# Performance work log

Hardware: AMD Instinct MI355X
Metric: run time of the kernel (lower is better)

## Reference

```python
import jax, jax.numpy as jnp
import numpy as np

H = 8          # n_heads
D = 1024       # dim_tgt == dim_mem
DQ = D // H    # per-head dim = 128
BN = 512       # LFFN bottleneck (hardcoded in module)
HID = 1024     # LFFN hidden (hardcoded in module)
B = 16
S_T = 1024     # target length
S_M = 2048     # memory length
SCALE = DQ ** 0.25  # module uses dim_q ** (1/4)
EPS = 1e-5


def _ln(x, g, b):
    m = jnp.mean(x, axis=-1, keepdims=True)
    v = jnp.mean(jnp.square(x - m), axis=-1, keepdims=True)
    return (x - m) * jax.lax.rsqrt(v + EPS) * g + b


def _mhla(xq, xk, xv, Wq, Wk, Wv, Wo, masked):
    # per-head projections: x [b,s,D] x W [H,D,DQ] -> [b,H,s,DQ]
    Q = jnp.einsum('bsq,hqd->bhsd', xq, Wq)
    K = jnp.einsum('bsq,hqd->bhsd', xk, Wk)
    V = jnp.einsum('bsq,hqd->bhsd', xv, Wv)
    if masked:
        s, d = Q.shape[-2], Q.shape[-1]
        # module adds log(triu(ones).T) directly to Q: 0 where d_idx<=t, -inf otherwise
        m = jnp.where(jnp.arange(d)[None, :] <= jnp.arange(s)[:, None], 0.0, -jnp.inf)
        Q = Q + m.astype(Q.dtype)
    # softmax_col(K^T/d_k) over head-dim axis == softmax(K/d_k, axis=-1)
    A = jnp.einsum('bhsd,bhse->bhde', jax.nn.softmax(K / SCALE, axis=-1), V)  # [b,H,DQ,DQ]
    Bm = jnp.einsum('bhsd,bhde->bhse', jax.nn.softmax(Q / SCALE, axis=-1), A)  # [b,H,s,DQ]
    b, h, w, dd = Bm.shape
    # torch .view(b, w, h*d) on contiguous [b,h,w,d]: raw row-major reshape (no transpose)
    Bm = Bm.reshape(b, w, h * dd)
    return Bm @ Wo.T


def setup_inputs():
    key = jax.random.key(0)
    ks = jax.random.split(key, 24)
    r = lambda k, sh, s=0.02: (jax.random.normal(k, sh, jnp.float32) * s)
    return {
        'mem': jax.random.normal(ks[0], (B, S_M, D), jnp.float32),
        'y': jax.random.normal(ks[1], (B, S_T, D), jnp.float32),
        # self-attention (masked)
        'Wq1': r(ks[2], (H, D, DQ)), 'Wk1': r(ks[3], (H, D, DQ)), 'Wv1': r(ks[4], (H, D, DQ)),
        'Wo1': r(ks[5], (D, D)),
        # cross-attention with memory
        'Wq2': r(ks[6], (H, D, DQ)), 'Wk2': r(ks[7], (H, D, DQ)), 'Wv2': r(ks[8], (H, D, DQ)),
        'Wo2': r(ks[9], (D, D)),
        # LFFN (torch Linear weights are [out, in])
        'E1': r(ks[10], (BN, D)), 'D1': r(ks[11], (HID, BN)),
        'E2': r(ks[12], (BN, HID)), 'D2': r(ks[13], (D, BN)),
        # LayerNorm affine params
        'g1': jnp.ones((D,), jnp.float32), 'b1': jnp.zeros((D,), jnp.float32),
        'g2': jnp.ones((D,), jnp.float32), 'b2': jnp.zeros((D,), jnp.float32),
        'g3': jnp.ones((D,), jnp.float32), 'b3': jnp.zeros((D,), jnp.float32),
    }


def reference(mem, y, Wq1, Wk1, Wv1, Wo1, Wq2, Wk2, Wv2, Wo2,
              E1, D1, E2, D2, g1, b1, g2, b2, g3, b3):
    # dropout layers are identity in eval mode
    y = y + _mhla(y, y, y, Wq1, Wk1, Wv1, Wo1, masked=True)
    y = _ln(y, g1, b1)
    y = y + _mhla(y, mem, mem, Wq2, Wk2, Wv2, Wo2, masked=False)
    y = _ln(y, g2, b2)
    # LFFN: E1 -> D1 -> swish -> E2 -> D2
    h = (y @ E1.T) @ D1.T
    h = h * jax.nn.sigmoid(h)
    ffn = (h @ E2.T) @ D2.T
    y = _ln(y + ffn, g3, b3)
    return y
```

## Files before the change

### kernel.cpp

```cpp
#include <hip/hip_runtime.h>
#include <hip/hip_bf16.h>

#define DEVI __device__ __forceinline__

typedef __bf16 bfrag __attribute__((ext_vector_type(8)));
typedef unsigned short us8 __attribute__((ext_vector_type(8)));
typedef float f32x4 __attribute__((ext_vector_type(4)));
typedef unsigned short ushort_t;

static constexpr int NB  = 16;
static constexpr int NH  = 8;
static constexpr int DIM = 1024;
static constexpr int DQh = 128;
static constexpr int ST  = 1024;
static constexpr int SM  = 2048;
static constexpr float INV_SCALE = 0.29730177875068026f;
static constexpr float LN_EPS = 1e-5f;

DEVI ushort_t f2bf(float f) {
  __hip_bfloat16 h = __float2bfloat16(f);
  return __builtin_bit_cast(ushort_t, h);
}
DEVI float bf2f(ushort_t u) {
  return __bfloat162float(__builtin_bit_cast(__hip_bfloat16, u));
}
DEVI bfrag ldfrag(const ushort_t* p) {
  return __builtin_bit_cast(bfrag, *(const us8*)p);
}
DEVI void gl16(const ushort_t* g, ushort_t* l) {
  __builtin_amdgcn_global_load_lds(
      (const __attribute__((address_space(1))) void*)g,
      (__attribute__((address_space(3))) void*)l, 16, 0, 0);
}

enum { ST_BF16 = 0, ST_SWISH = 1, ST_F32RES = 2, ST_SCR = 3, ST_QKV = 4 };

template<int STORE>
__global__ __launch_bounds__(256, 2)
void gemm_bb(const ushort_t* __restrict__ A, const ushort_t* __restrict__ Bt,
             const float* __restrict__ Res,
             ushort_t* __restrict__ Q0, ushort_t* __restrict__ Q1,
             ushort_t* __restrict__ Q2, float* __restrict__ Cf,
             int M, int N, int K, long aZ, long bZ, int logS)
{
  __shared__ ushort_t As[128][32];
  __shared__ ushort_t Bs[128][32];
  const int tid = threadIdx.x;
  int bx = blockIdx.x, by = blockIdx.y;
  if (gridDim.z == 1) {
    const int gx = gridDim.x;
    const int nwg = gx * gridDim.y;
    int bid = by * gx + bx;
    if ((nwg & 7) == 0) bid = (bid & 7) * (nwg >> 3) + (bid >> 3);
    bx = bid % gx; by = bid / gx;
  }
  const int z = blockIdx.z;
  const int m0 = by * 128, n0 = bx * 128;
  A  += aZ * (long)z;
  Bt += bZ * (long)z;

  const int lane = tid & 63;
  const int w = tid >> 6;
  const int wr = (w >> 1) * 64, wc = (w & 1) * 64;
  const int frow = lane & 15;

  const int grow = lane >> 2;
  const int gk = ((lane & 3) ^ ((lane >> 3) & 3)) * 8;
  const ushort_t* Ag = A + (long)(m0 + w * 32 + grow) * K + gk;
  const ushort_t* Bg = Bt + (long)(n0 + w * 32 + grow) * K + gk;

  f32x4 acc[4][4];
  #pragma unroll
  for (int i = 0; i < 4; ++i)
    #pragma unroll
    for (int j = 0; j < 4; ++j) acc[i][j] = f32x4{0.f, 0.f, 0.f, 0.f};

  const int kqs = ((frow >> 1) & 3);
  for (int k0 = 0; k0 < K; k0 += 32) {
    __syncthreads();
    gl16(Ag + k0,               &As[w * 32][0]);
    gl16(Ag + k0 + (long)16 * K, &As[w * 32 + 16][0]);
    gl16(Bg + k0,               &Bs[w * 32][0]);
    gl16(Bg + k0 + (long)16 * K, &Bs[w * 32 + 16][0]);
    __syncthreads();
    const int kq = (lane >> 4) ^ kqs;
    bfrag af[4], bf[4];
    #pragma unroll
    for (int i = 0; i < 4; ++i) af[i] = ldfrag(&As[wr + i * 16 + frow][kq * 8]);
    #pragma unroll
    for (int j = 0; j < 4; ++j) bf[j] = ldfrag(&Bs[wc + j * 16 + frow][kq * 8]);
    #pragma unroll
    for (int i = 0; i < 4; ++i)
      #pragma unroll
      for (int j = 0; j < 4; ++j)
        acc[i][j] = __builtin_amdgcn_mfma_f32_16x16x32_bf16(af[i], bf[j], acc[i][j], 0, 0, 0);
  }

  const int rb = (lane >> 4) * 4;
  if constexpr (STORE == ST_QKV) {
    const int sel = n0 >> 10;
    const int h = (n0 >> 7) & 7;
    ushort_t* __restrict__ Bq = (sel == 0) ? Q0 : ((sel == 1) ? Q1 : Q2);
    const int S = 1 << logS;
    #pragma unroll
    for (int i = 0; i < 4; ++i)
      #pragma unroll
      for (int j = 0; j < 4; ++j)
        #pragma unroll
        for (int e = 0; e < 4; ++e) {
          const int gm = m0 + wr + i * 16 + rb + e;
          const int dq = wc + j * 16 + frow;
          const int b = gm >> logS, s = gm & (S - 1);
          Bq[((long)(h * 16 + b) * S + (long)s) * 128 + dq] = f2bf(acc[i][j][e]);
        }
  } else {
    #pragma unroll
    for (int i = 0; i < 4; ++i)
      #pragma unroll
      for (int j = 0; j < 4; ++j)
        #pragma unroll
        for (int e = 0; e < 4; ++e) {
          const int gm = m0 + wr + i * 16 + rb + e;
          const int gn = n0 + wc + j * 16 + frow;
          float val = acc[i][j][e];
          if constexpr (STORE == ST_SWISH) val = val / (1.0f + __expf(-val));
          if constexpr (STORE == ST_BF16 || STORE == ST_SWISH) {
            Q0[(long)gm * N + gn] = f2bf(val);
          } else if constexpr (STORE == ST_F32RES) {
            Cf[(long)gm * N + gn] = val + Res[(long)gm * N + gn];
          } else if constexpr (STORE == ST_SCR) {
            const int b = z & 15, hh = z >> 4;
            Q0[(long)b * (ST * DIM) + (long)(hh * 128 + (gm >> 3)) * DIM +
               (gm & 7) * 128 + gn] = f2bf(val);
          }
        }
  }
}

__global__ __launch_bounds__(256, 2)
void gemm_ktv(const ushort_t* __restrict__ Kp, const ushort_t* __restrict__ Vp,
              ushort_t* __restrict__ AT, int S)
{
  __shared__ ushort_t As[128][40];
  __shared__ ushort_t Bs[128][40];
  const int tid = threadIdx.x;
  const int z = blockIdx.x;
  const ushort_t* Vb = Vp + (long)z * S * DQh;
  const ushort_t* Kb = Kp + (long)z * S * DQh;
  const int lane = tid & 63;
  const int wr = ((tid >> 6) >> 1) * 64, wc = ((tid >> 6) & 1) * 64;
  const int frow = lane & 15, fk = (lane >> 4) * 8;
  const int c = tid & 127;
  const int sr0 = tid >> 7;

  f32x4 acc[4][4];
  #pragma unroll
  for (int i = 0; i < 4; ++i)
    #pragma unroll
    for (int j = 0; j < 4; ++j) acc[i][j] = f32x4{0.f, 0.f, 0.f, 0.f};

  for (int s0 = 0; s0 < S; s0 += 32) {
    __syncthreads();
    #pragma unroll
    for (int p = 0; p < 16; ++p) {
      const int sr = sr0 + p * 2;
      As[c][sr] = Vb[(long)(s0 + sr) * DQh + c];
      Bs[c][sr] = Kb[(long)(s0 + sr) * DQh + c];
    }
    __syncthreads();
    bfrag af[4], bfv[4];
    #pragma unroll
    for (int i = 0; i < 4; ++i) af[i]  = ldfrag(&As[wr + i * 16 + frow][fk]);
    #pragma unroll
    for (int j = 0; j < 4; ++j) bfv[j] = ldfrag(&Bs[wc + j * 16 + frow][fk]);
    #pragma unroll
    for (int i = 0; i < 4; ++i)
      #pragma unroll
      for (int j = 0; j < 4; ++j)
        acc[i][j] = __builtin_amdgcn_mfma_f32_16x16x32_bf16(af[i], bfv[j], acc[i][j], 0, 0, 0);
  }
  const int rb = (lane >> 4) * 4;
  #pragma unroll
  for (int i = 0; i < 4; ++i)
    #pragma unroll
    for (int j = 0; j < 4; ++j)
      #pragma unroll
      for (int e = 0; e < 4; ++e)
        AT[(long)z * 16384 + (long)(wr + i * 16 + rb + e) * 128 + (wc + j * 16 + frow)] =
            f2bf(acc[i][j][e]);
}

template<bool MASKED>
__global__ __launch_bounds__(256)
void softmax128(ushort_t* __restrict__ X, int smask)
{
  const int row = blockIdx.x * 4 + (threadIdx.x >> 6);
  const int lane = threadIdx.x & 63;
  ushort_t* xr = X + (long)row * 128;
  float x0 = bf2f(xr[lane]) * INV_SCALE;
  float x1 = bf2f(xr[lane + 64]) * INV_SCALE;
  if constexpr (MASKED) {
    const int s = row & smask;
    if (lane > s)      x0 = -3.0e38f;
    if (lane + 64 > s) x1 = -3.0e38f;
  }
  float mx = fmaxf(x0, x1);
  #pragma unroll
  for (int o = 32; o; o >>= 1) mx = fmaxf(mx, __shfl_xor(mx, o));
  const float e0 = __expf(x0 - mx);
  const float e1 = __expf(x1 - mx);
  float sm = e0 + e1;
  #pragma unroll
  for (int o = 32; o; o >>= 1) sm += __shfl_xor(sm, o);
  const float inv = 1.0f / sm;
  xr[lane]      = f2bf(e0 * inv);
  xr[lane + 64] = f2bf(e1 * inv);
}

__global__ __launch_bounds__(256)
void layernorm_k(const float* __restrict__ X, const float* __restrict__ G,
                 const float* __restrict__ Bta, float* __restrict__ Y,
                 ushort_t* __restrict__ Yb)
{
  const int row = blockIdx.x;
  const int t = threadIdx.x;
  const float4 v = *(const float4*)(X + (long)row * DIM + t * 4);
  float s  = v.x + v.y + v.z + v.w;
  float sq = v.x * v.x + v.y * v.y + v.z * v.z + v.w * v.w;
  #pragma unroll
  for (int o = 32; o; o >>= 1) { s += __shfl_xor(s, o); sq += __shfl_xor(sq, o); }
  __shared__ float ps[4], pq[4];
  if ((t & 63) == 0) { ps[t >> 6] = s; pq[t >> 6] = sq; }
  __syncthreads();
  s  = ps[0] + ps[1] + ps[2] + ps[3];
  sq = pq[0] + pq[1] + pq[2] + pq[3];
  const float mean = s * (1.0f / DIM);
  const float var  = sq * (1.0f / DIM) - mean * mean;
  const float rstd = rsqrtf(var + LN_EPS);
  const float4 gv = *(const float4*)(G + t * 4);
  const float4 bv = *(const float4*)(Bta + t * 4);
  float4 o;
  o.x = (v.x - mean) * rstd * gv.x + bv.x;
  o.y = (v.y - mean) * rstd * gv.y + bv.y;
  o.z = (v.z - mean) * rstd * gv.z + bv.z;
  o.w = (v.w - mean) * rstd * gv.w + bv.w;
  *(float4*)(Y + (long)row * DIM + t * 4) = o;
  if (Yb) {
    ushort4 ob = make_ushort4(f2bf(o.x), f2bf(o.y), f2bf(o.z), f2bf(o.w));
    *(ushort4*)(Yb + (long)row * DIM + t * 4) = ob;
  }
}

__global__ __launch_bounds__(256)
void transpose_cast(const float* __restrict__ W, ushort_t* __restrict__ Wt)
{
  __shared__ float tile[32][33];
  const int z = blockIdx.z;
  const int kb = blockIdx.y * 32;
  const int nb = blockIdx.x * 32;
  const float* src = W + (long)z * DIM * DQh;
  ushort_t* dst = Wt + (long)z * DIM * DQh;
  const int tx = threadIdx.x & 31;
  const int ty = threadIdx.x >> 5;
  #pragma unroll
  for (int r = 0; r < 32; r += 8)
    tile[ty + r][tx] = src[(long)(kb + ty + r) * DQh + nb + tx];
  __syncthreads();
  #pragma unroll
  for (int r = 0; r < 32; r += 8)
    dst[(long)(nb + ty + r) * DIM + kb + tx] = f2bf(tile[tx][ty + r]);
}

__global__ __launch_bounds__(256)
void cast_bf16(const float* __restrict__ X, ushort_t* __restrict__ Yq)
{
  const long i = ((long)blockIdx.x * 256 + threadIdx.x) * 4;
  const float4 v = *(const float4*)(X + i);
  ushort4 sv = make_ushort4(f2bf(v.x), f2bf(v.y), f2bf(v.z), f2bf(v.w));
  *(ushort4*)(Yq + i) = sv;
}


extern "C" void kernel_launch(void* const* d_in, const int* in_sizes, int n_in,
                              void* d_out, int out_size, void* d_ws, size_t ws_size,
                              hipStream_t stream)
{
  (void)in_sizes; (void)n_in; (void)out_size; (void)ws_size;
  const float* mem = (const float*)d_in[0];
  const float* y0  = (const float*)d_in[1];
  const float* Wq1 = (const float*)d_in[2];
  const float* Wk1 = (const float*)d_in[3];
  const float* Wv1 = (const float*)d_in[4];
  const float* Wo1 = (const float*)d_in[5];
  const float* Wq2 = (const float*)d_in[6];
  const float* Wk2 = (const float*)d_in[7];
  const float* Wv2 = (const float*)d_in[8];
  const float* Wo2 = (const float*)d_in[9];
  const float* E1  = (const float*)d_in[10];
  const float* D1  = (const float*)d_in[11];
  const float* E2  = (const float*)d_in[12];
  const float* D2  = (const float*)d_in[13];
  const float* g1  = (const float*)d_in[14];
  const float* b1  = (const float*)d_in[15];
  const float* g2  = (const float*)d_in[16];
  const float* b2  = (const float*)d_in[17];
  const float* g3  = (const float*)d_in[18];
  const float* b3  = (const float*)d_in[19];

  char* ws = (char*)d_ws;
  const size_t MB = 1ull << 20;
  ushort_t* wcat1 = (ushort_t*)(ws + 0 * MB);
  ushort_t* wkv2  = (ushort_t*)(ws + 6 * MB);
  ushort_t* wq2t  = (ushort_t*)(ws + 10 * MB);
  ushort_t* wo1b  = (ushort_t*)(ws + 12 * MB);
  ushort_t* wo2b  = (ushort_t*)(ws + 14 * MB);
  ushort_t* e1b   = (ushort_t*)(ws + 16 * MB);
  ushort_t* d1b   = (ushort_t*)(ws + 17 * MB);
  ushort_t* e2b   = (ushort_t*)(ws + 18 * MB);
  ushort_t* d2b   = (ushort_t*)(ws + 19 * MB);
  ushort_t* y0b   = (ushort_t*)(ws + 20 * MB);
  ushort_t* memb  = (ushort_t*)(ws + 52 * MB);
  ushort_t* qbuf  = (ushort_t*)(ws + 116 * MB);
  ushort_t* kbuf  = (ushort_t*)(ws + 148 * MB);
  ushort_t* vbuf  = (ushort_t*)(ws + 212 * MB);
  ushort_t* amatT = (ushort_t*)(ws + 276 * MB);
  ushort_t* attnb = (ushort_t*)(ws + 280 * MB);
  float*    ybuf  = (float*)(ws + 312 * MB);
  ushort_t* ybf   = (ushort_t*)(ws + 376 * MB);
  ushort_t* hbuf  = (ushort_t*)(ws + 408 * MB);
  ushort_t* bn1   = attnb;
  ushort_t* bn2   = qbuf;

  cast_bf16<<<16384, 256, 0, stream>>>(y0, y0b);
  cast_bf16<<<32768, 256, 0, stream>>>(mem, memb);
  transpose_cast<<<dim3(4, 32, 8), 256, 0, stream>>>(Wq1, wcat1);
  transpose_cast<<<dim3(4, 32, 8), 256, 0, stream>>>(Wk1, wcat1 + (1 << 20));
  transpose_cast<<<dim3(4, 32, 8), 256, 0, stream>>>(Wv1, wcat1 + (2 << 20));
  transpose_cast<<<dim3(4, 32, 8), 256, 0, stream>>>(Wk2, wkv2);
  transpose_cast<<<dim3(4, 32, 8), 256, 0, stream>>>(Wv2, wkv2 + (1 << 20));
  transpose_cast<<<dim3(4, 32, 8), 256, 0, stream>>>(Wq2, wq2t);
  cast_bf16<<<1024, 256, 0, stream>>>(Wo1, wo1b);
  cast_bf16<<<1024, 256, 0, stream>>>(Wo2, wo2b);
  cast_bf16<<<512, 256, 0, stream>>>(E1, e1b);
  cast_bf16<<<512, 256, 0, stream>>>(D1, d1b);
  cast_bf16<<<512, 256, 0, stream>>>(E2, e2b);
  cast_bf16<<<512, 256, 0, stream>>>(D2, d2b);

  gemm_bb<ST_QKV><<<dim3(24, 128, 1), 256, 0, stream>>>(
      y0b, wcat1, nullptr, qbuf, kbuf, vbuf, nullptr,
      NB * ST, 3072, DIM, 0, 0, 10);
  softmax128<true><<<NH * NB * ST / 4, 256, 0, stream>>>(qbuf, ST - 1);
  softmax128<false><<<NH * NB * ST / 4, 256, 0, stream>>>(kbuf, 0);
  gemm_ktv<<<NH * NB, 256, 0, stream>>>(kbuf, vbuf, amatT, ST);
  gemm_bb<ST_SCR><<<dim3(1, 8, 128), 256, 0, stream>>>(
      qbuf, amatT, nullptr, attnb, nullptr, nullptr, nullptr,
      ST, DQh, DQh, (long)ST * DQh, 16384, 0);
  gemm_bb<ST_F32RES><<<dim3(8, 128, 1), 256, 0, stream>>>(
      attnb, wo1b, y0, nullptr, nullptr, nullptr, ybuf,
      NB * ST, DIM, DIM, 0, 0, 0);
  layernorm_k<<<NB * ST, 256, 0, stream>>>(ybuf, g1, b1, ybuf, ybf);

  gemm_bb<ST_QKV><<<dim3(8, 128, 1), 256, 0, stream>>>(
      ybf, wq2t, nullptr, qbuf, nullptr, nullptr, nullptr,
      NB * ST, 1024, DIM, 0, 0, 10);
  gemm_bb<ST_QKV><<<dim3(16, 256, 1), 256, 0, stream>>>(
      memb, wkv2, nullptr, kbuf, vbuf, nullptr, nullptr,
      NB * SM, 2048, DIM, 0, 0, 11);
  softmax128<false><<<NH * NB * ST / 4, 256, 0, stream>>>(qbuf, 0);
  softmax128<false><<<NH * NB * SM / 4, 256, 0, stream>>>(kbuf, 0);
  gemm_ktv<<<NH * NB, 256, 0, stream>>>(kbuf, vbuf, amatT, SM);
  gemm_bb<ST_SCR><<<dim3(1, 8, 128), 256, 0, stream>>>(
      qbuf, amatT, nullptr, attnb, nullptr, nullptr, nullptr,
      ST, DQh, DQh, (long)ST * DQh, 16384, 0);
  gemm_bb<ST_F32RES><<<dim3(8, 128, 1), 256, 0, stream>>>(
      attnb, wo2b, ybuf, nullptr, nullptr, nullptr, ybuf,
      NB * ST, DIM, DIM, 0, 0, 0);
  layernorm_k<<<NB * ST, 256, 0, stream>>>(ybuf, g2, b2, ybuf, ybf);

  gemm_bb<ST_BF16><<<dim3(4, 128, 1), 256, 0, stream>>>(
      ybf, e1b, nullptr, bn1, nullptr, nullptr, nullptr,
      NB * ST, 512, DIM, 0, 0, 0);
  gemm_bb<ST_SWISH><<<dim3(8, 128, 1), 256, 0, stream>>>(
      bn1, d1b, nullptr, hbuf, nullptr, nullptr, nullptr,
      NB * ST, DIM, 512, 0, 0, 0);
  gemm_bb<ST_BF16><<<dim3(4, 128, 1), 256, 0, stream>>>(
      hbuf, e2b, nullptr, bn2, nullptr, nullptr, nullptr,
      NB * ST, 512, DIM, 0, 0, 0);
  gemm_bb<ST_F32RES><<<dim3(8, 128, 1), 256, 0, stream>>>(
      bn2, d2b, ybuf, nullptr, nullptr, nullptr, ybuf,
      NB * ST, DIM, 512, 0, 0, 0);
  layernorm_k<<<NB * ST, 256, 0, stream>>>(ybuf, g3, b3, (float*)d_out, nullptr);
}
```

Baseline: 1.007 ms.

## Add 256x256 multi-stage pipelined GEMM kernel for large projection GEMMs

Adds a 512-thread GEMM with a 256x256 output tile and a four-slot LDS ring fed by global_load_lds. Each block keeps up to three k-slices in flight, using vmcnt waits, barriers and s_setprio to overlap loads with MFMA work. The kernel is used for the QKV, output-projection, D1-swish and D2-residual GEMMs, while the narrower N=512 and attention GEMMs stay on the old 128x128 kernel. The larger tile raises arithmetic intensity and hides load latency, at the cost of high register and LDS use, one block per CU, and fewer blocks for wave balance.

```diff
diff --git a/kernel.cpp b/kernel.cpp
--- a/kernel.cpp
+++ b/kernel.cpp
@@ -36,12 +36,136 @@
 enum { ST_BF16 = 0, ST_SWISH = 1, ST_F32RES = 2, ST_SCR = 3, ST_QKV = 4 };
 
 template<int STORE>
+__global__ __launch_bounds__(512)
+void gemm256(const ushort_t* __restrict__ A, const ushort_t* __restrict__ Bt,
+             const float* __restrict__ Res,
+             ushort_t* __restrict__ P0, ushort_t* __restrict__ P1,
+             ushort_t* __restrict__ P2, float* __restrict__ Cf,
+             int M, int N, int K, int logS)
+{
+  __shared__ ushort_t Asl[4][8192];
+  __shared__ ushort_t Bsl[4][8192];
+  const int tid = threadIdx.x;
+  int bx = blockIdx.x, by = blockIdx.y;
+  {
+    const int gx = gridDim.x;
+    const int nwg = gx * gridDim.y;
+    int bid = by * gx + bx;
+    if ((nwg & 7) == 0) bid = (bid & 7) * (nwg >> 3) + (bid >> 3);
+    bx = bid % gx; by = bid / gx;
+  }
+  const int m0 = by * 256, n0 = bx * 256;
+
+  const int lane = tid & 63;
+  const int w  = tid >> 6;
+  const int wm = w >> 2;
+  const int wn = w & 3;
+  const int frow = lane & 15;
+  const int q    = lane >> 4;
+  const int swz  = (frow >> 1) & 3;
+
+  const ushort_t* Ab = A + (long)m0 * K;
+  const ushort_t* Bb = Bt + (long)n0 * K;
+
+  const int sr0 = w * 32 + (lane >> 2);
+  const int sg  = ((lane & 3) ^ ((lane >> 3) & 3)) * 8;
+  const int ld0 = w * 1024;
+
+  f32x4 acc[8][4];
+  #pragma unroll
+  for (int i = 0; i < 8; ++i)
+    #pragma unroll
+    for (int j = 0; j < 4; ++j) acc[i][j] = f32x4{0.f, 0.f, 0.f, 0.f};
+
+  auto STG = [&](const ushort_t* G, int koff, ushort_t* unit) {
+    gl16(G + (long)sr0 * K + koff + sg,        unit + ld0);
+    gl16(G + (long)(sr0 + 16) * K + koff + sg, unit + ld0 + 512);
+  };
+
+  STG(Ab, 0,  Asl[0]); STG(Bb, 0,  Bsl[0]);
+  STG(Ab, 32, Asl[1]); STG(Bb, 32, Bsl[1]);
+  STG(Ab, 64, Asl[2]); STG(Bb, 64, Bsl[2]);
+  asm volatile("s_waitcnt vmcnt(4)" ::: "memory");
+  __builtin_amdgcn_s_barrier();
+
+  const int nk = K >> 6;
+  for (int t = 0; t < nk; t += 2) {
+    bfrag bf[4];
+    #pragma unroll
+    for (int ph = 0; ph < 8; ++ph) {
+      const int tpar = (ph >> 2) & 1;
+      const int kh   = (ph >> 1) & 1;
+      const int mh   = ph & 1;
+      const ushort_t* Au = Asl[tpar * 2 + kh];
+      const ushort_t* Bu = Bsl[tpar * 2 + kh];
+      bfrag af[4];
+      if (mh == 0) {
+        #pragma unroll
+        for (int j = 0; j < 4; ++j)
+          bf[j] = ldfrag(Bu + (wn * 64 + j * 16 + frow) * 32 + ((q ^ swz) * 8));
+      }
+      #pragma unroll
+      for (int i = 0; i < 4; ++i)
+        af[i] = ldfrag(Au + (wm * 128 + mh * 64 + i * 16 + frow) * 32 + ((q ^ swz) * 8));
+
+      if (ph == 0) STG(Ab, (t + 1) * 64 + 32, Asl[3]);
+      if (ph == 1) STG(Bb, (t + 1) * 64 + 32, Bsl[3]);
+      if (ph == 2 && t + 2 < nk) STG(Ab, (t + 2) * 64,      Asl[0]);
+      if (ph == 3 && t + 2 < nk) STG(Bb, (t + 2) * 64,      Bsl[0]);
+      if (ph == 4 && t + 2 < nk) STG(Ab, (t + 2) * 64 + 32, Asl[1]);
+      if (ph == 5 && t + 2 < nk) STG(Bb, (t + 2) * 64 + 32, Bsl[1]);
+      if (ph == 6 && t + 3 < nk) STG(Ab, (t + 3) * 64,      Asl[2]);
+      if (ph == 7 && t + 3 < nk) STG(Bb, (t + 3) * 64,      Bsl[2]);
+
+      if (ph == 3 || ph == 7) asm volatile("s_waitcnt vmcnt(4)" ::: "memory");
+      __builtin_amdgcn_s_barrier();
+      __builtin_amdgcn_s_setprio(1);
+      #pragma unroll
+      for (int i = 0; i < 4; ++i)
+        #pragma unroll
+        for (int j = 0; j < 4; ++j)
+          acc[mh * 4 + i][j] =
+              __builtin_amdgcn_mfma_f32_16x16x32_bf16(af[i], bf[j], acc[mh * 4 + i][j], 0, 0, 0);
+      __builtin_amdgcn_s_setprio(0);
+      __builtin_amdgcn_s_barrier();
+    }
+  }
+
+  const int rb = (lane >> 4) * 4;
+  #pragma unroll
+  for (int mf = 0; mf < 8; ++mf) {
+    #pragma unroll
+    for (int j = 0; j < 4; ++j) {
+      #pragma unroll
+      for (int e = 0; e < 4; ++e) {
+        const int gm = m0 + wm * 128 + mf * 16 + rb + e;
+        const int gn = n0 + wn * 64 + j * 16 + frow;
+        float val = acc[mf][j][e];
+        if constexpr (STORE == ST_SWISH) val = val / (1.0f + __expf(-val));
+        if constexpr (STORE == ST_BF16 || STORE == ST_SWISH) {
+          P0[(long)gm * N + gn] = f2bf(val);
+        } else if constexpr (STORE == ST_F32RES) {
+          Cf[(long)gm * N + gn] = val + Res[(long)gm * N + gn];
+        } else if constexpr (STORE == ST_QKV) {
+          const int sel = gn >> 10;
+          const int h   = (gn >> 7) & 7;
+          const int dq  = gn & 127;
+          ushort_t* Bq = (sel == 0) ? P0 : ((sel == 1) ? P1 : P2);
+          const int S = 1 << logS;
+          const int b = gm >> logS, s = gm & (S - 1);
+          Bq[((long)(h * 16 + b) * S + (long)s) * 128 + dq] = f2bf(val);
+        }
+      }
+    }
+  }
+}
+
+template<int STORE>
 __global__ __launch_bounds__(256, 2)
 void gemm_bb(const ushort_t* __restrict__ A, const ushort_t* __restrict__ Bt,
              const float* __restrict__ Res,
-             ushort_t* __restrict__ Q0, ushort_t* __restrict__ Q1,
-             ushort_t* __restrict__ Q2, float* __restrict__ Cf,
-             int M, int N, int K, long aZ, long bZ, int logS)
+             ushort_t* __restrict__ Q0, float* __restrict__ Cf,
+             int M, int N, int K, long aZ, long bZ)
 {
   __shared__ ushort_t As[128][32];
   __shared__ ushort_t Bs[128][32];
@@ -78,9 +202,9 @@
   const int kqs = ((frow >> 1) & 3);
   for (int k0 = 0; k0 < K; k0 += 32) {
     __syncthreads();
-    gl16(Ag + k0,               &As[w * 32][0]);
+    gl16(Ag + k0,                &As[w * 32][0]);
     gl16(Ag + k0 + (long)16 * K, &As[w * 32 + 16][0]);
-    gl16(Bg + k0,               &Bs[w * 32][0]);
+    gl16(Bg + k0,                &Bs[w * 32][0]);
     gl16(Bg + k0 + (long)16 * K, &Bs[w * 32 + 16][0]);
     __syncthreads();
     const int kq = (lane >> 4) ^ kqs;
@@ -97,43 +221,26 @@
   }
 
   const int rb = (lane >> 4) * 4;
-  if constexpr (STORE == ST_QKV) {
-    const int sel = n0 >> 10;
-    const int h = (n0 >> 7) & 7;
-    ushort_t* __restrict__ Bq = (sel == 0) ? Q0 : ((sel == 1) ? Q1 : Q2);
-    const int S = 1 << logS;
-    #pragma unroll
-    for (int i = 0; i < 4; ++i)
-      #pragma unroll
-      for (int j = 0; j < 4; ++j)
-        #pragma unroll
-        for (int e = 0; e < 4; ++e) {
-          const int gm = m0 + wr + i * 16 + rb + e;
-          const int dq = wc + j * 16 + frow;
-          const int b = gm >> logS, s = gm & (S - 1);
-          Bq[((long)(h * 16 + b) * S + (long)s) * 128 + dq] = f2bf(acc[i][j][e]);
+  #pragma unroll
+  for (int i = 0; i < 4; ++i) {
+    #pragma unroll
+    for (int j = 0; j < 4; ++j) {
+      #pragma unroll
+      for (int e = 0; e < 4; ++e) {
+        const int gm = m0 + wr + i * 16 + rb + e;
+        const int gn = n0 + wc + j * 16 + frow;
+        float val = acc[i][j][e];
+        if constexpr (STORE == ST_BF16) {
+          Q0[(long)gm * N + gn] = f2bf(val);
+        } else if constexpr (STORE == ST_F32RES) {
+          Cf[(long)gm * N + gn] = val + Res[(long)gm * N + gn];
+        } else if constexpr (STORE == ST_SCR) {
+          const int b = z & 15, hh = z >> 4;
+          Q0[(long)b * (ST * DIM) + (long)(hh * 128 + (gm >> 3)) * DIM +
+             (gm & 7) * 128 + gn] = f2bf(val);
         }
-  } else {
-    #pragma unroll
-    for (int i = 0; i < 4; ++i)
-      #pragma unroll
-      for (int j = 0; j < 4; ++j)
-        #pragma unroll
-        for (int e = 0; e < 4; ++e) {
-          const int gm = m0 + wr + i * 16 + rb + e;
-          const int gn = n0 + wc + j * 16 + frow;
-          float val = acc[i][j][e];
-          if constexpr (STORE == ST_SWISH) val = val / (1.0f + __expf(-val));
-          if constexpr (STORE == ST_BF16 || STORE == ST_SWISH) {
-            Q0[(long)gm * N + gn] = f2bf(val);
-          } else if constexpr (STORE == ST_F32RES) {
-            Cf[(long)gm * N + gn] = val + Res[(long)gm * N + gn];
-          } else if constexpr (STORE == ST_SCR) {
-            const int b = z & 15, hh = z >> 4;
-            Q0[(long)b * (ST * DIM) + (long)(hh * 128 + (gm >> 3)) * DIM +
-               (gm & 7) * 128 + gn] = f2bf(val);
-          }
-        }
+      }
+    }
   }
 }
 
@@ -346,48 +453,37 @@
   cast_bf16<<<512, 256, 0, stream>>>(E2, e2b);
   cast_bf16<<<512, 256, 0, stream>>>(D2, d2b);
 
-  gemm_bb<ST_QKV><<<dim3(24, 128, 1), 256, 0, stream>>>(
-      y0b, wcat1, nullptr, qbuf, kbuf, vbuf, nullptr,
-      NB * ST, 3072, DIM, 0, 0, 10);
+  gemm256<ST_QKV><<<dim3(12, 64), 512, 0, stream>>>(
+      y0b, wcat1, nullptr, qbuf, kbuf, vbuf, nullptr, NB * ST, 3072, DIM, 10);
   softmax128<true><<<NH * NB * ST / 4, 256, 0, stream>>>(qbuf, ST - 1);
   softmax128<false><<<NH * NB * ST / 4, 256, 0, stream>>>(kbuf, 0);
   gemm_ktv<<<NH * NB, 256, 0, stream>>>(kbuf, vbuf, amatT, ST);
   gemm_bb<ST_SCR><<<dim3(1, 8, 128), 256, 0, stream>>>(
-      qbuf, amatT, nullptr, attnb, nullptr, nullptr, nullptr,
-      ST, DQh, DQh, (long)ST * DQh, 16384, 0);
-  gemm_bb<ST_F32RES><<<dim3(8, 128, 1), 256, 0, stream>>>(
-      attnb, wo1b, y0, nullptr, nullptr, nullptr, ybuf,
-      NB * ST, DIM, DIM, 0, 0, 0);
+      qbuf, amatT, nullptr, attnb, nullptr, ST, DQh, DQh, (long)ST * DQh, 16384);
+  gemm256<ST_F32RES><<<dim3(4, 64), 512, 0, stream>>>(
+      attnb, wo1b, y0, nullptr, nullptr, nullptr, ybuf, NB * ST, DIM, DIM, 0);
   layernorm_k<<<NB * ST, 256, 0, stream>>>(ybuf, g1, b1, ybuf, ybf);
 
-  gemm_bb<ST_QKV><<<dim3(8, 128, 1), 256, 0, stream>>>(
-      ybf, wq2t, nullptr, qbuf, nullptr, nullptr, nullptr,
-      NB * ST, 1024, DIM, 0, 0, 10);
-  gemm_bb<ST_QKV><<<dim3(16, 256, 1), 256, 0, stream>>>(
-      memb, wkv2, nullptr, kbuf, vbuf, nullptr, nullptr,
-      NB * SM, 2048, DIM, 0, 0, 11);
+  gemm256<ST_QKV><<<dim3(4, 64), 512, 0, stream>>>(
+      ybf, wq2t, nullptr, qbuf, nullptr, nullptr, nullptr, NB * ST, 1024, DIM, 10);
+  gemm256<ST_QKV><<<dim3(8, 128), 512, 0, stream>>>(
+      memb, wkv2, nullptr, kbuf, vbuf, nullptr, nullptr, NB * SM, 2048, DIM, 11);
   softmax128<false><<<NH * NB * ST / 4, 256, 0, stream>>>(qbuf, 0);
   softmax128<false><<<NH * NB * SM / 4, 256, 0, stream>>>(kbuf, 0);
   gemm_ktv<<<NH * NB, 256, 0, stream>>>(kbuf, vbuf, amatT, SM);
   gemm_bb<ST_SCR><<<dim3(1, 8, 128), 256, 0, stream>>>(
-      qbuf, amatT, nullptr, attnb, nullptr, nullptr, nullptr,
-      ST, DQh, DQh, (long)ST * DQh, 16384, 0);
-  gemm_bb<ST_F32RES><<<dim3(8, 128, 1), 256, 0, stream>>>(
-      attnb, wo2b, ybuf, nullptr, nullptr, nullptr, ybuf,
-      NB * ST, DIM, DIM, 0, 0, 0);
+      qbuf, amatT, nullptr, attnb, nullptr, ST, DQh, DQh, (long)ST * DQh, 16384);
+  gemm256<ST_F32RES><<<dim3(4, 64), 512, 0, stream>>>(
+      attnb, wo2b, ybuf, nullptr, nullptr, nullptr, ybuf, NB * ST, DIM, DIM, 0);
   layernorm_k<<<NB * ST, 256, 0, stream>>>(ybuf, g2, b2, ybuf, ybf);
 
   gemm_bb<ST_BF16><<<dim3(4, 128, 1), 256, 0, stream>>>(
-      ybf, e1b, nullptr, bn1, nullptr, nullptr, nullptr,
-      NB * ST, 512, DIM, 0, 0, 0);
-  gemm_bb<ST_SWISH><<<dim3(8, 128, 1), 256, 0, stream>>>(
-      bn1, d1b, nullptr, hbuf, nullptr, nullptr, nullptr,
-      NB * ST, DIM, 512, 0, 0, 0);
+      ybf, e1b, nullptr, bn1, nullptr, NB * ST, 512, DIM, 0, 0);
+  gemm256<ST_SWISH><<<dim3(4, 64), 512, 0, stream>>>(
+      bn1, d1b, nullptr, hbuf, nullptr, nullptr, nullptr, NB * ST, DIM, 512, 0);
   gemm_bb<ST_BF16><<<dim3(4, 128, 1), 256, 0, stream>>>(
-      hbuf, e2b, nullptr, bn2, nullptr, nullptr, nullptr,
-      NB * ST, 512, DIM, 0, 0, 0);
-  gemm_bb<ST_F32RES><<<dim3(8, 128, 1), 256, 0, stream>>>(
-      bn2, d2b, ybuf, nullptr, nullptr, nullptr, ybuf,
-      NB * ST, DIM, 512, 0, 0, 0);
+      hbuf, e2b, nullptr, bn2, nullptr, NB * ST, 512, DIM, 0, 0);
+  gemm256<ST_F32RES><<<dim3(4, 64), 512, 0, stream>>>(
+      bn2, d2b, ybuf, nullptr, nullptr, nullptr, ybuf, NB * ST, DIM, 512, 0);
   layernorm_k<<<NB * ST, 256, 0, stream>>>(ybuf, g3, b3, (float*)d_out, nullptr);
 }
```

Result: no change. 1.022 ms (+1.5%).

## Fuse head-dim softmax into QKV GEMM epilogue and split K^T V over sequence

Applied to the files above, without the earlier changes.

Adds a gemm_qkv kernel whose waves each own full 128-wide head rows, so the scaled, optionally causal-masked softmax over the head dimension is applied in registers before storing Q/K, removing the separate softmax passes. gemm_ktv is split across sequence chunks writing fp32 partials, followed by a ktv_reduce kernel, to raise parallelism beyond 128 blocks. This trades extra partial-sum traffic, and a different wave tiling with fewer MFMAs per B-fragment load, for fewer memory round trips and better CU utilization.

```diff
diff --git a/kernel.cpp b/kernel.cpp
--- a/kernel.cpp
+++ b/kernel.cpp
@@ -33,15 +33,115 @@
       (__attribute__((address_space(3))) void*)l, 16, 0, 0);
 }
 
-enum { ST_BF16 = 0, ST_SWISH = 1, ST_F32RES = 2, ST_SCR = 3, ST_QKV = 4 };
+enum { ST_BF16 = 0, ST_SWISH = 1, ST_F32RES = 2, ST_SCR = 3 };
+
+__global__ __launch_bounds__(256, 4)
+void gemm_qkv(const ushort_t* __restrict__ A, const ushort_t* __restrict__ Bt,
+              ushort_t* __restrict__ P0, ushort_t* __restrict__ P1,
+              ushort_t* __restrict__ P2,
+              int M, int N, int K, int logS, int smflags, int maskflags)
+{
+  __shared__ ushort_t As[128][32];
+  __shared__ ushort_t Bs[128][32];
+  const int tid = threadIdx.x;
+  int bx = blockIdx.x, by = blockIdx.y;
+  {
+    const int gx = gridDim.x;
+    const int nwg = gx * gridDim.y;
+    int bid = by * gx + bx;
+    if ((nwg & 7) == 0) bid = (bid & 7) * (nwg >> 3) + (bid >> 3);
+    bx = bid % gx; by = bid / gx;
+  }
+  const int m0 = by * 128, n0 = bx * 128;
+
+  const int lane = tid & 63;
+  const int w = tid >> 6;
+  const int wr = w * 32;
+  const int frow = lane & 15;
+  const int q = lane >> 4;
+
+  const int grow = lane >> 2;
+  const int gk = ((lane & 3) ^ ((lane >> 3) & 3)) * 8;
+  const ushort_t* Ag = A + (long)(m0 + w * 32 + grow) * K + gk;
+  const ushort_t* Bg = Bt + (long)(n0 + w * 32 + grow) * K + gk;
+
+  f32x4 acc[2][8];
+  #pragma unroll
+  for (int i = 0; i < 2; ++i)
+    #pragma unroll
+    for (int j = 0; j < 8; ++j) acc[i][j] = f32x4{0.f, 0.f, 0.f, 0.f};
+
+  const int kqs = (frow >> 1) & 3;
+  for (int k0 = 0; k0 < K; k0 += 32) {
+    __syncthreads();
+    gl16(Ag + k0,                &As[w * 32][0]);
+    gl16(Ag + k0 + (long)16 * K, &As[w * 32 + 16][0]);
+    gl16(Bg + k0,                &Bs[w * 32][0]);
+    gl16(Bg + k0 + (long)16 * K, &Bs[w * 32 + 16][0]);
+    __syncthreads();
+    const int kq = (q ^ kqs) * 8;
+    const bfrag af0 = ldfrag(&As[wr + frow][kq]);
+    const bfrag af1 = ldfrag(&As[wr + 16 + frow][kq]);
+    #pragma unroll
+    for (int j = 0; j < 8; ++j) {
+      const bfrag bf = ldfrag(&Bs[j * 16 + frow][kq]);
+      acc[0][j] = __builtin_amdgcn_mfma_f32_16x16x32_bf16(af0, bf, acc[0][j], 0, 0, 0);
+      acc[1][j] = __builtin_amdgcn_mfma_f32_16x16x32_bf16(af1, bf, acc[1][j], 0, 0, 0);
+    }
+  }
+
+  const int sel = n0 >> 10;
+  const bool dosm   = (smflags >> sel) & 1;
+  const bool domask = (maskflags >> sel) & 1;
+  const int h = (n0 >> 7) & 7;
+  ushort_t* __restrict__ Bq = (sel == 0) ? P0 : ((sel == 1) ? P1 : P2);
+  const int S = 1 << logS;
+  #pragma unroll
+  for (int i = 0; i < 2; ++i) {
+    #pragma unroll
+    for (int e = 0; e < 4; ++e) {
+      const int gm = m0 + wr + i * 16 + q * 4 + e;
+      const int b = gm >> logS, s = gm & (S - 1);
+      float v[8];
+      #pragma unroll
+      for (int j = 0; j < 8; ++j) v[j] = acc[i][j][e];
+      if (dosm) {
+        #pragma unroll
+        for (int j = 0; j < 8; ++j) {
+          v[j] *= INV_SCALE;
+          if (domask && (j * 16 + frow) > s) v[j] = -3.0e38f;
+        }
+        float mx = v[0];
+        #pragma unroll
+        for (int j = 1; j < 8; ++j) mx = fmaxf(mx, v[j]);
+        mx = fmaxf(mx, __shfl_xor(mx, 1));
+        mx = fmaxf(mx, __shfl_xor(mx, 2));
+        mx = fmaxf(mx, __shfl_xor(mx, 4));
+        mx = fmaxf(mx, __shfl_xor(mx, 8));
+        float sm = 0.f;
+        #pragma unroll
+        for (int j = 0; j < 8; ++j) { v[j] = __expf(v[j] - mx); sm += v[j]; }
+        sm += __shfl_xor(sm, 1);
+        sm += __shfl_xor(sm, 2);
+        sm += __shfl_xor(sm, 4);
+        sm += __shfl_xor(sm, 8);
+        const float inv = 1.0f / sm;
+        #pragma unroll
+        for (int j = 0; j < 8; ++j) v[j] *= inv;
+      }
+      ushort_t* rowp = Bq + ((long)(h * 16 + b) * S + (long)s) * 128;
+      #pragma unroll
+      for (int j = 0; j < 8; ++j) rowp[j * 16 + frow] = f2bf(v[j]);
+    }
+  }
+}
 
 template<int STORE>
 __global__ __launch_bounds__(256, 2)
 void gemm_bb(const ushort_t* __restrict__ A, const ushort_t* __restrict__ Bt,
              const float* __restrict__ Res,
-             ushort_t* __restrict__ Q0, ushort_t* __restrict__ Q1,
-             ushort_t* __restrict__ Q2, float* __restrict__ Cf,
-             int M, int N, int K, long aZ, long bZ, int logS)
+             ushort_t* __restrict__ P0, float* __restrict__ Cf,
+             int M, int N, int K, long aZ, long bZ)
 {
   __shared__ ushort_t As[128][32];
   __shared__ ushort_t Bs[128][32];
@@ -63,6 +163,7 @@
   const int w = tid >> 6;
   const int wr = (w >> 1) * 64, wc = (w & 1) * 64;
   const int frow = lane & 15;
+  const int q = lane >> 4;
 
   const int grow = lane >> 2;
   const int gk = ((lane & 3) ^ ((lane >> 3) & 3)) * 8;
@@ -75,20 +176,20 @@
     #pragma unroll
     for (int j = 0; j < 4; ++j) acc[i][j] = f32x4{0.f, 0.f, 0.f, 0.f};
 
-  const int kqs = ((frow >> 1) & 3);
+  const int kqs = (frow >> 1) & 3;
   for (int k0 = 0; k0 < K; k0 += 32) {
     __syncthreads();
-    gl16(Ag + k0,               &As[w * 32][0]);
+    gl16(Ag + k0,                &As[w * 32][0]);
     gl16(Ag + k0 + (long)16 * K, &As[w * 32 + 16][0]);
-    gl16(Bg + k0,               &Bs[w * 32][0]);
+    gl16(Bg + k0,                &Bs[w * 32][0]);
     gl16(Bg + k0 + (long)16 * K, &Bs[w * 32 + 16][0]);
     __syncthreads();
-    const int kq = (lane >> 4) ^ kqs;
+    const int kq = (q ^ kqs) * 8;
     bfrag af[4], bf[4];
     #pragma unroll
-    for (int i = 0; i < 4; ++i) af[i] = ldfrag(&As[wr + i * 16 + frow][kq * 8]);
-    #pragma unroll
-    for (int j = 0; j < 4; ++j) bf[j] = ldfrag(&Bs[wc + j * 16 + frow][kq * 8]);
+    for (int i = 0; i < 4; ++i) af[i] = ldfrag(&As[wr + i * 16 + frow][kq]);
+    #pragma unroll
+    for (int j = 0; j < 4; ++j) bf[j] = ldfrag(&Bs[wc + j * 16 + frow][kq]);
     #pragma unroll
     for (int i = 0; i < 4; ++i)
       #pragma unroll
@@ -96,57 +197,43 @@
         acc[i][j] = __builtin_amdgcn_mfma_f32_16x16x32_bf16(af[i], bf[j], acc[i][j], 0, 0, 0);
   }
 
-  const int rb = (lane >> 4) * 4;
-  if constexpr (STORE == ST_QKV) {
-    const int sel = n0 >> 10;
-    const int h = (n0 >> 7) & 7;
-    ushort_t* __restrict__ Bq = (sel == 0) ? Q0 : ((sel == 1) ? Q1 : Q2);
-    const int S = 1 << logS;
-    #pragma unroll
-    for (int i = 0; i < 4; ++i)
-      #pragma unroll
-      for (int j = 0; j < 4; ++j)
-        #pragma unroll
-        for (int e = 0; e < 4; ++e) {
-          const int gm = m0 + wr + i * 16 + rb + e;
-          const int dq = wc + j * 16 + frow;
-          const int b = gm >> logS, s = gm & (S - 1);
-          Bq[((long)(h * 16 + b) * S + (long)s) * 128 + dq] = f2bf(acc[i][j][e]);
+  const int rb = q * 4;
+  #pragma unroll
+  for (int i = 0; i < 4; ++i) {
+    #pragma unroll
+    for (int j = 0; j < 4; ++j) {
+      #pragma unroll
+      for (int e = 0; e < 4; ++e) {
+        const int gm = m0 + wr + i * 16 + rb + e;
+        const int gn = n0 + wc + j * 16 + frow;
+        float val = acc[i][j][e];
+        if constexpr (STORE == ST_SWISH) val = val / (1.0f + __expf(-val));
+        if constexpr (STORE == ST_F32RES) {
+          Cf[(long)gm * N + gn] = val + Res[(long)gm * N + gn];
+        } else if constexpr (STORE == ST_SCR) {
+          const int b = z & 15, hh = z >> 4;
+          P0[(long)b * (ST * DIM) + (long)(hh * 128 + (gm >> 3)) * DIM +
+             (gm & 7) * 128 + gn] = f2bf(val);
+        } else {
+          P0[(long)gm * N + gn] = f2bf(val);
         }
-  } else {
-    #pragma unroll
-    for (int i = 0; i < 4; ++i)
-      #pragma unroll
-      for (int j = 0; j < 4; ++j)
-        #pragma unroll
-        for (int e = 0; e < 4; ++e) {
-          const int gm = m0 + wr + i * 16 + rb + e;
-          const int gn = n0 + wc + j * 16 + frow;
-          float val = acc[i][j][e];
-          if constexpr (STORE == ST_SWISH) val = val / (1.0f + __expf(-val));
-          if constexpr (STORE == ST_BF16 || STORE == ST_SWISH) {
-            Q0[(long)gm * N + gn] = f2bf(val);
-          } else if constexpr (STORE == ST_F32RES) {
-            Cf[(long)gm * N + gn] = val + Res[(long)gm * N + gn];
-          } else if constexpr (STORE == ST_SCR) {
-            const int b = z & 15, hh = z >> 4;
-            Q0[(long)b * (ST * DIM) + (long)(hh * 128 + (gm >> 3)) * DIM +
-               (gm & 7) * 128 + gn] = f2bf(val);
-          }
-        }
+      }
+    }
   }
 }
 
 __global__ __launch_bounds__(256, 2)
 void gemm_ktv(const ushort_t* __restrict__ Kp, const ushort_t* __restrict__ Vp,
-              ushort_t* __restrict__ AT, int S)
+              float* __restrict__ P, int S, int SC)
 {
   __shared__ ushort_t As[128][40];
   __shared__ ushort_t Bs[128][40];
   const int tid = threadIdx.x;
   const int z = blockIdx.x;
-  const ushort_t* Vb = Vp + (long)z * S * DQh;
-  const ushort_t* Kb = Kp + (long)z * S * DQh;
+  const int ch = blockIdx.y;
+  const long base = ((long)z * S + (long)ch * SC) * DQh;
+  const ushort_t* Vb = Vp + base;
+  const ushort_t* Kb = Kp + base;
   const int lane = tid & 63;
   const int wr = ((tid >> 6) >> 1) * 64, wc = ((tid >> 6) & 1) * 64;
   const int frow = lane & 15, fk = (lane >> 4) * 8;
@@ -159,7 +246,7 @@
     #pragma unroll
     for (int j = 0; j < 4; ++j) acc[i][j] = f32x4{0.f, 0.f, 0.f, 0.f};
 
-  for (int s0 = 0; s0 < S; s0 += 32) {
+  for (int s0 = 0; s0 < SC; s0 += 32) {
     __syncthreads();
     #pragma unroll
     for (int p = 0; p < 16; ++p) {
@@ -179,6 +266,7 @@
       for (int j = 0; j < 4; ++j)
         acc[i][j] = __builtin_amdgcn_mfma_f32_16x16x32_bf16(af[i], bfv[j], acc[i][j], 0, 0, 0);
   }
+  float* Pz = P + ((long)ch * 128 + z) * 16384;
   const int rb = (lane >> 4) * 4;
   #pragma unroll
   for (int i = 0; i < 4; ++i)
@@ -186,35 +274,20 @@
     for (int j = 0; j < 4; ++j)
       #pragma unroll
       for (int e = 0; e < 4; ++e)
-        AT[(long)z * 16384 + (long)(wr + i * 16 + rb + e) * 128 + (wc + j * 16 + frow)] =
-            f2bf(acc[i][j][e]);
-}
-
-template<bool MASKED>
+        Pz[(long)(wr + i * 16 + rb + e) * 128 + (wc + j * 16 + frow)] = acc[i][j][e];
+}
+
 __global__ __launch_bounds__(256)
-void softmax128(ushort_t* __restrict__ X, int smask)
-{
-  const int row = blockIdx.x * 4 + (threadIdx.x >> 6);
-  const int lane = threadIdx.x & 63;
-  ushort_t* xr = X + (long)row * 128;
-  float x0 = bf2f(xr[lane]) * INV_SCALE;
-  float x1 = bf2f(xr[lane + 64]) * INV_SCALE;
-  if constexpr (MASKED) {
-    const int s = row & smask;
-    if (lane > s)      x0 = -3.0e38f;
-    if (lane + 64 > s) x1 = -3.0e38f;
-  }
-  float mx = fmaxf(x0, x1);
-  #pragma unroll
-  for (int o = 32; o; o >>= 1) mx = fmaxf(mx, __shfl_xor(mx, o));
-  const float e0 = __expf(x0 - mx);
-  const float e1 = __expf(x1 - mx);
-  float sm = e0 + e1;
-  #pragma unroll
-  for (int o = 32; o; o >>= 1) sm += __shfl_xor(sm, o);
-  const float inv = 1.0f / sm;
-  xr[lane]      = f2bf(e0 * inv);
-  xr[lane + 64] = f2bf(e1 * inv);
+void ktv_reduce(const float* __restrict__ P, ushort_t* __restrict__ AT, int nch)
+{
+  const long i = ((long)blockIdx.x * 256 + threadIdx.x) * 4;
+  float4 s = *(const float4*)(P + i);
+  for (int c = 1; c < nch; ++c) {
+    const float4 v = *(const float4*)(P + (long)c * 2097152 + i);
+    s.x += v.x; s.y += v.y; s.z += v.z; s.w += v.w;
+  }
+  ushort4 o = make_ushort4(f2bf(s.x), f2bf(s.y), f2bf(s.z), f2bf(s.w));
+  *(ushort4*)(AT + i) = o;
 }
 
 __global__ __launch_bounds__(256)
@@ -328,6 +401,7 @@
   float*    ybuf  = (float*)(ws + 312 * MB);
   ushort_t* ybf   = (ushort_t*)(ws + 376 * MB);
   ushort_t* hbuf  = (ushort_t*)(ws + 408 * MB);
+  float*    pbuf  = (float*)(ws + 440 * MB);
   ushort_t* bn1   = attnb;
   ushort_t* bn2   = qbuf;
 
@@ -346,48 +420,36 @@
   cast_bf16<<<512, 256, 0, stream>>>(E2, e2b);
   cast_bf16<<<512, 256, 0, stream>>>(D2, d2b);
 
-  gemm_bb<ST_QKV><<<dim3(24, 128, 1), 256, 0, stream>>>(
-      y0b, wcat1, nullptr, qbuf, kbuf, vbuf, nullptr,
-      NB * ST, 3072, DIM, 0, 0, 10);
-  softmax128<true><<<NH * NB * ST / 4, 256, 0, stream>>>(qbuf, ST - 1);
-  softmax128<false><<<NH * NB * ST / 4, 256, 0, stream>>>(kbuf, 0);
-  gemm_ktv<<<NH * NB, 256, 0, stream>>>(kbuf, vbuf, amatT, ST);
+  gemm_qkv<<<dim3(24, 128), 256, 0, stream>>>(
+      y0b, wcat1, qbuf, kbuf, vbuf, NB * ST, 3072, DIM,
+      10,  0b011,  0b001);
+  gemm_ktv<<<dim3(128, 2), 256, 0, stream>>>(kbuf, vbuf, pbuf, ST, 512);
+  ktv_reduce<<<2048, 256, 0, stream>>>(pbuf, amatT, 2);
   gemm_bb<ST_SCR><<<dim3(1, 8, 128), 256, 0, stream>>>(
-      qbuf, amatT, nullptr, attnb, nullptr, nullptr, nullptr,
-      ST, DQh, DQh, (long)ST * DQh, 16384, 0);
+      qbuf, amatT, nullptr, attnb, nullptr, ST, DQh, DQh, (long)ST * DQh, 16384);
   gemm_bb<ST_F32RES><<<dim3(8, 128, 1), 256, 0, stream>>>(
-      attnb, wo1b, y0, nullptr, nullptr, nullptr, ybuf,
-      NB * ST, DIM, DIM, 0, 0, 0);
+      attnb, wo1b, y0, nullptr, ybuf, NB * ST, DIM, DIM, 0, 0);
   layernorm_k<<<NB * ST, 256, 0, stream>>>(ybuf, g1, b1, ybuf, ybf);
 
-  gemm_bb<ST_QKV><<<dim3(8, 128, 1), 256, 0, stream>>>(
-      ybf, wq2t, nullptr, qbuf, nullptr, nullptr, nullptr,
-      NB * ST, 1024, DIM, 0, 0, 10);
-  gemm_bb<ST_QKV><<<dim3(16, 256, 1), 256, 0, stream>>>(
-      memb, wkv2, nullptr, kbuf, vbuf, nullptr, nullptr,
-      NB * SM, 2048, DIM, 0, 0, 11);
-  softmax128<false><<<NH * NB * ST / 4, 256, 0, stream>>>(qbuf, 0);
-  softmax128<false><<<NH * NB * SM / 4, 256, 0, stream>>>(kbuf, 0);
-  gemm_ktv<<<NH * NB, 256, 0, stream>>>(kbuf, vbuf, amatT, SM);
+  gemm_qkv<<<dim3(8, 128), 256, 0, stream>>>(
+      ybf, wq2t, qbuf, nullptr, nullptr, NB * ST, 1024, DIM, 10, 0b001, 0);
+  gemm_qkv<<<dim3(16, 256), 256, 0, stream>>>(
+      memb, wkv2, kbuf, vbuf, nullptr, NB * SM, 2048, DIM, 11, 0b001, 0);
+  gemm_ktv<<<dim3(128, 4), 256, 0, stream>>>(kbuf, vbuf, pbuf, SM, 512);
+  ktv_reduce<<<2048, 256, 0, stream>>>(pbuf, amatT, 4);
   gemm_bb<ST_SCR><<<dim3(1, 8, 128), 256, 0, stream>>>(
-      qbuf, amatT, nullptr, attnb, nullptr, nullptr, nullptr,
-      ST, DQh, DQh, (long)ST * DQh, 16384, 0);
+      qbuf, amatT, nullptr, attnb, nullptr, ST, DQh, DQh, (long)ST * DQh, 16384);
   gemm_bb<ST_F32RES><<<dim3(8, 128, 1), 256, 0, stream>>>(
-      attnb, wo2b, ybuf, nullptr, nullptr, nullptr, ybuf,
-      NB * ST, DIM, DIM, 0, 0, 0);
+      attnb, wo2b, ybuf, nullptr, ybuf, NB * ST, DIM, DIM, 0, 0);
   layernorm_k<<<NB * ST, 256, 0, stream>>>(ybuf, g2, b2, ybuf, ybf);
 
   gemm_bb<ST_BF16><<<dim3(4, 128, 1), 256, 0, stream>>>(
-      ybf, e1b, nullptr, bn1, nullptr, nullptr, nullptr,
-      NB * ST, 512, DIM, 0, 0, 0);
+      ybf, e1b, nullptr, bn1, nullptr, NB * ST, 512, DIM, 0, 0);
   gemm_bb<ST_SWISH><<<dim3(8, 128, 1), 256, 0, stream>>>(
-      bn1, d1b, nullptr, hbuf, nullptr, nullptr, nullptr,
-      NB * ST, DIM, 512, 0, 0, 0);
+      bn1, d1b, nullptr, hbuf, nullptr, NB * ST, DIM, 512, 0, 0);
   gemm_bb<ST_BF16><<<dim3(4, 128, 1), 256, 0, stream>>>(
-      hbuf, e2b, nullptr, bn2, nullptr, nullptr, nullptr,
-      NB * ST, 512, DIM, 0, 0, 0);
+      hbuf, e2b, nullptr, bn2, nullptr, NB * ST, 512, DIM, 0, 0);
   gemm_bb<ST_F32RES><<<dim3(8, 128, 1), 256, 0, stream>>>(
-      bn2, d2b, ybuf, nullptr, nullptr, nullptr, ybuf,
-      NB * ST, DIM, 512, 0, 0, 0);
+      bn2, d2b, ybuf, nullptr, ybuf, NB * ST, DIM, 512, 0, 0);
   layernorm_k<<<NB * ST, 256, 0, stream>>>(ybuf, g3, b3, (float*)d_out, nullptr);
 }
```

Measured after the change: 871.6 us. 13.4% less time.
